# Kernel optimization log

Hardware: AMD Instinct MI355X
Metric: run time of the kernel (lower is better)

Reference implementation:

```python
import jax, jax.numpy as jnp
import numpy as np

C = 256      # channels (multiple of 32 for GroupNorm)
K = 3        # kernel
PAD = 1      # padding
G = 32       # GroupNorm groups
EPS = 1e-5


def setup_inputs() -> dict:
    key = jax.random.key(0)
    ks = jax.random.split(key, 7)
    B, H, W = 4, 64, 64
    return {
        "x": jax.random.normal(ks[0], (B, C, H, W), jnp.float32),
        "offset": jax.random.normal(ks[1], (B, 2 * K * K, H, W), jnp.float32),
        "weight": jax.random.normal(ks[2], (C, C, K, K), jnp.float32) * 0.01,
        "att_w": jax.random.normal(ks[3], (1, C), jnp.float32) * 0.01,
        "att_b": jnp.zeros((1,), jnp.float32),
        "gamma": jnp.ones((C,), jnp.float32),
        "beta": jnp.zeros((C,), jnp.float32),
    }


def _bilinear_one(xb, py, px):
    # xb: [C, H, W]; py, px: [KK, H, W] fractional sample coords (zero-pad outside)
    H, W = xb.shape[1], xb.shape[2]
    y0 = jnp.floor(py)
    x0 = jnp.floor(px)
    y1 = y0 + 1.0
    x1 = x0 + 1.0
    wy1 = py - y0
    wy0 = 1.0 - wy1
    wx1 = px - x0
    wx0 = 1.0 - wx1

    def g(yi, xi):
        valid = (yi >= 0) & (yi < H) & (xi >= 0) & (xi < W)
        yc = jnp.clip(yi, 0, H - 1).astype(jnp.int32)
        xc = jnp.clip(xi, 0, W - 1).astype(jnp.int32)
        return xb[:, yc, xc] * valid[None].astype(xb.dtype)  # [C, KK, H, W]

    return (g(y0, x0) * (wy0 * wx0)[None] + g(y0, x1) * (wy0 * wx1)[None]
            + g(y1, x0) * (wy1 * wx0)[None] + g(y1, x1) * (wy1 * wx1)[None])


def reference(x, offset, weight, att_w, att_b, gamma, beta):
    B, Cc, H, W = x.shape
    KK = K * K
    off = offset.reshape(B, KK, 2, H, W)  # (dy, dx) per kernel tap
    ii, jj = jnp.meshgrid(jnp.arange(K), jnp.arange(K), indexing='ij')
    dky = (ii - PAD).reshape(KK).astype(x.dtype)
    dkx = (jj - PAD).reshape(KK).astype(x.dtype)
    ys = jnp.arange(H, dtype=x.dtype)
    xs = jnp.arange(W, dtype=x.dtype)
    # sample coords [B, KK, H, W]
    py = ys[None, :, None] + dky[:, None, None] + off[:, :, 0]
    px = xs[None, None, :] + dkx[:, None, None] + off[:, :, 1]

    # deformable unfold: [B, C, KK, H, W]
    xu = jax.vmap(_bilinear_one)(x, py, px)

    # max over kernel taps -> channel attention gate
    xm = xu.max(axis=2)  # [B, C, H, W]
    att = jax.nn.sigmoid(jnp.einsum('bchw,oc->bohw', xm, att_w)
                         + att_b[None, :, None, None])  # [B, 1, H, W]

    # gate the unfolded samples, then emulate the conv as one GEMM
    xw = xu * att[:, :, None]  # broadcast over C, KK
    cols = xw.transpose(1, 2, 0, 3, 4).reshape(Cc * KK, B * H * W)  # [C*KK, BHW]
    out = (weight.reshape(Cc, Cc * KK) @ cols).reshape(Cc, B, H, W).transpose(1, 0, 2, 3)

    # GroupNorm(32, C) + ReLU
    og = out.reshape(B, G, Cc // G, H, W)
    mu = og.mean(axis=(2, 3, 4), keepdims=True)
    var = og.var(axis=(2, 3, 4), keepdims=True)
    on = ((og - mu) * jax.lax.rsqrt(var + EPS)).reshape(B, Cc, H, W)
    return jax.nn.relu(on * gamma[None, :, None, None] + beta[None, :, None, None])
```

## Files before the change

kernel.cpp:

```cpp
#include <hip/hip_runtime.h>

#define CT 256
#define KDIM 2304
#define COLP 296

typedef unsigned short u16;
typedef _Float16 h2 __attribute__((ext_vector_type(2)));
typedef _Float16 h8 __attribute__((ext_vector_type(8)));
typedef __attribute__((ext_vector_type(4))) float f32x4;

__device__ __forceinline__ unsigned pkh(float a, float b) {
    h2 r; r[0] = (_Float16)a; r[1] = (_Float16)b;
    return __builtin_bit_cast(unsigned, r);
}

__device__ __forceinline__ void gload_lds16(const uint4* g, u16* l) {
    __builtin_amdgcn_global_load_lds((const __attribute__((address_space(1))) void*)g,
                                     (__attribute__((address_space(3))) void*)l, 16, 0, 0);
}

__global__ __launch_bounds__(256) void k_prep(const float* __restrict__ x, uint4* __restrict__ xi,
                                              const float* __restrict__ wgt, uint4* __restrict__ pw)
{
    if (blockIdx.x < 2048) {
        int u = blockIdx.x * 256 + threadIdx.x;
        int bcg = u >> 12, p = u & 4095;
        const float* xp = x + (((size_t)bcg) << 15) + p;
        unsigned r[4];
#pragma unroll
        for (int i = 0; i < 4; ++i)
            r[i] = pkh(xp[(size_t)(2 * i) << 12], xp[(size_t)(2 * i + 1) << 12]);
        uint4 o; o.x = r[0]; o.y = r[1]; o.z = r[2]; o.w = r[3];
        xi[u] = o;
    } else {
        int u = (blockIdx.x - 2048) * 256 + threadIdx.x;
        int kc = u >> 10, rm = u & 1023;
        int m = rm >> 2, j = rm & 3;
        int round = kc / 9, tap = kc - round * 9;
        const float* src = wgt + (size_t)m * KDIM + tap;
        int c0 = round * 32 + j * 8;
        unsigned q[4];
#pragma unroll
        for (int i = 0; i < 4; ++i)
            q[i] = pkh(src[(size_t)(c0 + 2 * i) * 9], src[(size_t)(c0 + 2 * i + 1) * 9]);
        uint4 o; o.x = q[0]; o.y = q[1]; o.z = q[2]; o.w = q[3];
        pw[u] = o;
    }
}

__device__ __forceinline__ void gather_one(int it2, int sp, int xsb, size_t gfall,
                                           const uint2* s_wt, const int2* s_off,
                                           const u16* Xs, u16* col,
                                           const uint4* __restrict__ xi, int rbase, int nw)
{
    int tap = it2 >> 5, nn = it2 & 31;
    uint2 wp = s_wt[it2];
    h2 w01 = __builtin_bit_cast(h2, wp.x);
    h2 w23 = __builtin_bit_cast(h2, wp.y);
    h2 wxp = (h2){w01[0], w01[0]}, wyp = (h2){w01[1], w01[1]};
    h2 wzp = (h2){w23[0], w23[0]}, wwp = (h2){w23[1], w23[1]};
    int2 of = s_off[it2];
    int P00 = of.x & 0xffff, P01 = (of.x >> 16) & 0xffff;
    int P10 = of.y & 0xffff, P11 = (of.y >> 16) & 0xffff;
    uint4 c00, c01, c10, c11;
    int Q;
    Q = P00 - rbase;
    if ((unsigned)Q < (unsigned)nw) c00 = *(const uint4*)&Xs[xsb + Q * 8]; else c00 = xi[gfall + P00];
    Q = P01 - rbase;
    if ((unsigned)Q < (unsigned)nw) c01 = *(const uint4*)&Xs[xsb + Q * 8]; else c01 = xi[gfall + P01];
    Q = P10 - rbase;
    if ((unsigned)Q < (unsigned)nw) c10 = *(const uint4*)&Xs[xsb + Q * 8]; else c10 = xi[gfall + P10];
    Q = P11 - rbase;
    if ((unsigned)Q < (unsigned)nw) c11 = *(const uint4*)&Xs[xsb + Q * 8]; else c11 = xi[gfall + P11];
    const unsigned* a00 = (const unsigned*)&c00;
    const unsigned* a01 = (const unsigned*)&c01;
    const unsigned* a10 = (const unsigned*)&c10;
    const unsigned* a11 = (const unsigned*)&c11;
    unsigned o[4];
#pragma unroll
    for (int q = 0; q < 4; ++q) {
        h2 r = wxp * __builtin_bit_cast(h2, a00[q]) + wyp * __builtin_bit_cast(h2, a01[q])
             + wzp * __builtin_bit_cast(h2, a10[q]) + wwp * __builtin_bit_cast(h2, a11[q]);
        o[q] = __builtin_bit_cast(unsigned, r);
    }
    uint4 ov; ov.x = o[0]; ov.y = o[1]; ov.z = o[2]; ov.w = o[3];
    *(uint4*)&col[nn * COLP + tap * 32 + sp * 8] = ov;
}

__global__ __launch_bounds__(512, 2) void k_main(const uint4* __restrict__ xi, const float* __restrict__ off,
                                                 const uint4* __restrict__ pw, const float* __restrict__ att_w,
                                                 const float* __restrict__ att_b,
                                                 float* __restrict__ outp, float* __restrict__ gnpart)
{
    __shared__ uint2 s_wt[288];
    __shared__ int2 s_off[288];
    __shared__ u16 Xs[4 * 6656];
    __shared__ u16 col[32 * COLP];
    __shared__ float s_att[32];

    int rowblk = blockIdx.x >> 1, half = blockIdx.x & 1;
    int b = rowblk >> 6, h = rowblk & 63, n0 = half * 32;
    int tid = threadIdx.x;
    int lane = tid & 63, w = tid >> 6;
    int l15 = lane & 15, kb = lane >> 4;
    int wm = w * 32;
    int nn_a = w * 4 + (lane >> 4);
    int ca = (lane & 15) * 2;

    for (int e = tid; e < 288; e += 512) {
        int kk = e >> 5, wl = e & 31;
        int ww_ = n0 + wl;
        int ky = kk / 3, kx = kk - ky * 3;
        float dy = off[((size_t)(b * 18 + 2 * kk) * 64 + h) * 64 + ww_];
        float dx = off[((size_t)(b * 18 + 2 * kk + 1) * 64 + h) * 64 + ww_];
        float py = (float)(h + ky - 1) + dy;
        float px = (float)(ww_ + kx - 1) + dx;
        float y0f = floorf(py), x0f = floorf(px);
        int y0 = (int)y0f, x0 = (int)x0f;
        float fy = py - y0f, fx = px - x0f;
        float vy0 = (y0 >= 0 && y0 < 64) ? 1.f : 0.f;
        float vy1 = (y0 >= -1 && y0 < 63) ? 1.f : 0.f;
        float vx0 = (x0 >= 0 && x0 < 64) ? 1.f : 0.f;
        float vx1 = (x0 >= -1 && x0 < 63) ? 1.f : 0.f;
        float w0 = (1.f - fy) * (1.f - fx) * vy0 * vx0;
        float w1 = (1.f - fy) * fx * vy0 * vx1;
        float w2 = fy * (1.f - fx) * vy1 * vx0;
        float w3 = fy * fx * vy1 * vx1;
        uint2 wp;
        wp.x = pkh(w0, w1);
        wp.y = pkh(w2, w3);
        int yc0 = min(max(y0, 0), 63), yc1 = min(max(y0 + 1, 0), 63);
        int xc0 = min(max(x0, 0), 63), xc1 = min(max(x0 + 1, 0), 63);
        s_wt[e] = wp;
        s_off[e] = make_int2((yc0 * 64 + xc0) | ((yc0 * 64 + xc1) << 16),
                             (yc1 * 64 + xc0) | ((yc1 * 64 + xc1) << 16));
    }

    int r0 = max(0, h - 6), r1 = min(63, h + 6);
    int nrows = r1 - r0 + 1, nw = nrows * 64, rbase = r0 * 64;
    size_t xib = (size_t)(b * 32) << 12;

    float att_acc = 0.f;
    f32x4 acc[2][2];
#pragma unroll
    for (int mt = 0; mt < 2; ++mt)
#pragma unroll
        for (int nt = 0; nt < 2; ++nt) acc[mt][nt] = (f32x4){0.f, 0.f, 0.f, 0.f};

    int pwoff[2];
#pragma unroll
    for (int mt = 0; mt < 2; ++mt) pwoff[mt] = (wm + mt * 16 + l15) * 4 + kb;

#pragma unroll
    for (int cgl = 0; cgl < 2; ++cgl)
        for (int e = tid; e < nw; e += 512)
            gload_lds16(&xi[xib + ((size_t)cgl << 12) + rbase + e], &Xs[(cgl * 6656 + e * 8)]);

    for (int stage = 0; stage < 16; ++stage) {
        int buf = stage & 1;
        int s2 = stage & 1;
        __syncthreads();
        if (stage < 15) {
            size_t nb = xib + ((size_t)((stage + 1) * 2) << 12) + rbase;
#pragma unroll
            for (int cgl = 0; cgl < 2; ++cgl)
                for (int e = tid; e < nw; e += 512)
                    gload_lds16(&xi[nb + ((size_t)cgl << 12) + e],
                                &Xs[(((buf ^ 1) * 2 + cgl) * 6656 + e * 8)]);
        }
        {
            int it = tid;
            int cgl = (it >= 288) ? 1 : 0;
            gather_one(it - cgl * 288, s2 * 2 + cgl, (buf * 2 + cgl) * 6656,
                       xib + ((size_t)(stage * 2 + cgl) << 12), s_wt, s_off, Xs, col, xi, rbase, nw);
            if (tid >= 448) {
                int it2 = tid + 64;
                gather_one(it2 - 288, s2 * 2 + 1, (buf * 2 + 1) * 6656,
                           xib + ((size_t)(stage * 2 + 1) << 12), s_wt, s_off, Xs, col, xi, rbase, nw);
            }
        }

        if (stage & 1) {
            int round = stage >> 1;
            __syncthreads();

            uint4 aa[4][2];
#pragma unroll
            for (int ts = 0; ts < 4; ++ts)
#pragma unroll
                for (int mt = 0; mt < 2; ++mt)
                    aa[ts][mt] = pw[(size_t)(round * 9 + ts) * 1024 + pwoff[mt]];

            {
                int sp = ca >> 3, co = ca & 7;
                const u16* base = &col[nn_a * COLP + sp * 8 + co];
                float m0 = -1e30f, m1 = -1e30f;
#pragma unroll
                for (int t = 0; t < 9; ++t) {
                    unsigned v = *(const unsigned*)(base + t * 32);
                    h2 vv = __builtin_bit_cast(h2, v);
                    m0 = fmaxf(m0, (float)vv[0]);
                    m1 = fmaxf(m1, (float)vv[1]);
                }
                int cb = round * 32 + ca;
                att_acc += att_w[cb] * m0 + att_w[cb + 1] * m1;
            }

#pragma unroll
            for (int ts = 0; ts < 9; ++ts) {
                h8 bf[2];
#pragma unroll
                for (int nt = 0; nt < 2; ++nt)
                    bf[nt] = *(const h8*)&col[(nt * 16 + l15) * COLP + ts * 32 + kb * 8];
                h8 af[2];
#pragma unroll
                for (int mt = 0; mt < 2; ++mt) af[mt] = __builtin_bit_cast(h8, aa[ts & 3][mt]);
                if (ts + 4 < 9) {
#pragma unroll
                    for (int mt = 0; mt < 2; ++mt)
                        aa[ts & 3][mt] = pw[(size_t)(round * 9 + ts + 4) * 1024 + pwoff[mt]];
                }
#pragma unroll
                for (int mt = 0; mt < 2; ++mt)
#pragma unroll
                    for (int nt = 0; nt < 2; ++nt)
                        acc[mt][nt] = __builtin_amdgcn_mfma_f32_16x16x32_f16(af[mt], bf[nt], acc[mt][nt], 0, 0, 0);
            }
        }
    }

#pragma unroll
    for (int d = 1; d <= 8; d <<= 1) att_acc += __shfl_xor(att_acc, d);
    if ((lane & 15) == 0) s_att[nn_a] = 1.f / (1.f + expf(-(att_acc + att_b[0])));
    __syncthreads();

    float attn[2];
#pragma unroll
    for (int nt = 0; nt < 2; ++nt) attn[nt] = s_att[nt * 16 + l15];

#pragma unroll
    for (int mt = 0; mt < 2; ++mt) {
        float s1 = 0.f, s2 = 0.f;
#pragma unroll
        for (int nt = 0; nt < 2; ++nt)
#pragma unroll
            for (int r = 0; r < 4; ++r) {
                float v = acc[mt][nt][r] * attn[nt];
                int m = wm + mt * 16 + kb * 4 + r;
                outp[(((size_t)(b * CT + m)) << 12) + h * 64 + n0 + nt * 16 + l15] = v;
                s1 += v; s2 += v * v;
            }
#pragma unroll
        for (int d = 1; d <= 16; d <<= 1) {
            s1 += __shfl_xor(s1, d);
            s2 += __shfl_xor(s2, d);
        }
        if ((lane & 31) == 0) {
            int gidx = w * 4 + mt * 2 + (kb >> 1);
            gnpart[blockIdx.x * 64 + gidx * 2] = s1;
            gnpart[blockIdx.x * 64 + gidx * 2 + 1] = s2;
        }
    }
}

__global__ __launch_bounds__(256) void k_gn(const float* __restrict__ gnpart, const float* __restrict__ gamma,
                                            const float* __restrict__ beta, float* __restrict__ outp)
{
    __shared__ float rs1[128], rs2[128];
    __shared__ float s_stat[2];
    int bg = blockIdx.x;
    int b = bg >> 5, g = bg & 31;
    int tid = threadIdx.x;
    if (tid < 128) {
        int blk = (b * 64 + (tid >> 1)) * 2 + (tid & 1);
        rs1[tid] = gnpart[blk * 64 + g * 2];
        rs2[tid] = gnpart[blk * 64 + g * 2 + 1];
    }
    __syncthreads();
    if (tid < 64) {
        float a = rs1[tid] + rs1[tid + 64];
        float c = rs2[tid] + rs2[tid + 64];
#pragma unroll
        for (int d = 1; d <= 32; d <<= 1) {
            a += __shfl_xor(a, d);
            c += __shfl_xor(c, d);
        }
        if (tid == 0) {
            float mean = a * (1.f / 32768.f);
            float var = c * (1.f / 32768.f) - mean * mean;
            s_stat[0] = mean;
            s_stat[1] = rsqrtf(var + 1e-5f);
        }
    }
    __syncthreads();
    float mean = s_stat[0], rstd = s_stat[1];
    float4* p4 = (float4*)(outp + ((size_t)(b * CT + g * 8) << 12));
    for (int i = tid; i < 8192; i += 256) {
        int c = g * 8 + (i >> 10);
        float ga = gamma[c], be = beta[c];
        float4 v = p4[i];
        float4 r;
        r.x = fmaxf((v.x - mean) * rstd * ga + be, 0.f);
        r.y = fmaxf((v.y - mean) * rstd * ga + be, 0.f);
        r.z = fmaxf((v.z - mean) * rstd * ga + be, 0.f);
        r.w = fmaxf((v.w - mean) * rstd * ga + be, 0.f);
        p4[i] = r;
    }
}

extern "C" void kernel_launch(void* const* d_in, const int* in_sizes, int n_in,
                              void* d_out, int out_size, void* d_ws, size_t ws_size,
                              hipStream_t stream)
{
    const float* x = (const float*)d_in[0];
    const float* off = (const float*)d_in[1];
    const float* wgt = (const float*)d_in[2];
    const float* attw = (const float*)d_in[3];
    const float* attb = (const float*)d_in[4];
    const float* gamma = (const float*)d_in[5];
    const float* beta = (const float*)d_in[6];
    float* outp = (float*)d_out;

    char* ws = (char*)d_ws;
    uint4* xi = (uint4*)ws;
    uint4* pw = (uint4*)(ws + 8388608);
    float* gnpart = (float*)(ws + 9568256);

    k_prep<<<dim3(2336), dim3(256), 0, stream>>>(x, xi, wgt, pw);
    k_main<<<dim3(512), dim3(512), 0, stream>>>(xi, off, pw, attw, attb, outp, gnpart);
    k_gn<<<dim3(128), dim3(256), 0, stream>>>(gnpart, gamma, beta, outp);
}
```

Before: 147.1 us.

## Retile MFMA warps to 64x16 with single B fragment per step

Changes each warp's output tile from 32x32 (2x2 MFMA tiles) to 64 output channels by 16 pixels (4x1 tiles), so each step reads one column fragment from LDS but four weight fragments from global memory. Weight prefetch depth goes from 4 to 3 steps. GroupNorm partial sums are now written per 8 groups per warp with a doubled stride, and k_gn is rewritten to reduce 128 partials per group with wave shuffles. This trades LDS reads for more global weight loads and more registers.

```diff
diff --git a/kernel.cpp b/kernel.cpp
--- a/kernel.cpp
+++ b/kernel.cpp
@@ -103,7 +103,8 @@
     int tid = threadIdx.x;
     int lane = tid & 63, w = tid >> 6;
     int l15 = lane & 15, kb = lane >> 4;
-    int wm = w * 32;
+    int wm = (w & 3) * 64;
+    int nt_w = w >> 2;
     int nn_a = w * 4 + (lane >> 4);
     int ca = (lane & 15) * 2;
 
@@ -141,15 +142,14 @@
     size_t xib = (size_t)(b * 32) << 12;
 
     float att_acc = 0.f;
-    f32x4 acc[2][2];
-#pragma unroll
-    for (int mt = 0; mt < 2; ++mt)
-#pragma unroll
-        for (int nt = 0; nt < 2; ++nt) acc[mt][nt] = (f32x4){0.f, 0.f, 0.f, 0.f};
-
-    int pwoff[2];
-#pragma unroll
-    for (int mt = 0; mt < 2; ++mt) pwoff[mt] = (wm + mt * 16 + l15) * 4 + kb;
+    f32x4 acc[4];
+#pragma unroll
+    for (int mt = 0; mt < 4; ++mt) acc[mt] = (f32x4){0.f, 0.f, 0.f, 0.f};
+
+    int pwoff[4];
+#pragma unroll
+    for (int mt = 0; mt < 4; ++mt) pwoff[mt] = (wm + mt * 16 + l15) * 4 + kb;
+    int bcol = (nt_w * 16 + l15) * COLP + kb * 8;
 
 #pragma unroll
     for (int cgl = 0; cgl < 2; ++cgl)
@@ -184,11 +184,11 @@
             int round = stage >> 1;
             __syncthreads();
 
-            uint4 aa[4][2];
-#pragma unroll
-            for (int ts = 0; ts < 4; ++ts)
-#pragma unroll
-                for (int mt = 0; mt < 2; ++mt)
+            uint4 aa[3][4];
+#pragma unroll
+            for (int ts = 0; ts < 3; ++ts)
+#pragma unroll
+                for (int mt = 0; mt < 4; ++mt)
                     aa[ts][mt] = pw[(size_t)(round * 9 + ts) * 1024 + pwoff[mt]];
 
             {
@@ -208,23 +208,18 @@
 
 #pragma unroll
             for (int ts = 0; ts < 9; ++ts) {
-                h8 bf[2];
-#pragma unroll
-                for (int nt = 0; nt < 2; ++nt)
-                    bf[nt] = *(const h8*)&col[(nt * 16 + l15) * COLP + ts * 32 + kb * 8];
-                h8 af[2];
-#pragma unroll
-                for (int mt = 0; mt < 2; ++mt) af[mt] = __builtin_bit_cast(h8, aa[ts & 3][mt]);
-                if (ts + 4 < 9) {
-#pragma unroll
-                    for (int mt = 0; mt < 2; ++mt)
-                        aa[ts & 3][mt] = pw[(size_t)(round * 9 + ts + 4) * 1024 + pwoff[mt]];
+                h8 bf = *(const h8*)&col[bcol + ts * 32];
+                h8 af[4];
+#pragma unroll
+                for (int mt = 0; mt < 4; ++mt) af[mt] = __builtin_bit_cast(h8, aa[ts % 3][mt]);
+                if (ts + 3 < 9) {
+#pragma unroll
+                    for (int mt = 0; mt < 4; ++mt)
+                        aa[ts % 3][mt] = pw[(size_t)(round * 9 + ts + 3) * 1024 + pwoff[mt]];
                 }
 #pragma unroll
-                for (int mt = 0; mt < 2; ++mt)
-#pragma unroll
-                    for (int nt = 0; nt < 2; ++nt)
-                        acc[mt][nt] = __builtin_amdgcn_mfma_f32_16x16x32_f16(af[mt], bf[nt], acc[mt][nt], 0, 0, 0);
+                for (int mt = 0; mt < 4; ++mt)
+                    acc[mt] = __builtin_amdgcn_mfma_f32_16x16x32_f16(af[mt], bf, acc[mt], 0, 0, 0);
             }
         }
     }
@@ -234,31 +229,27 @@
     if ((lane & 15) == 0) s_att[nn_a] = 1.f / (1.f + expf(-(att_acc + att_b[0])));
     __syncthreads();
 
-    float attn[2];
-#pragma unroll
-    for (int nt = 0; nt < 2; ++nt) attn[nt] = s_att[nt * 16 + l15];
-
-#pragma unroll
-    for (int mt = 0; mt < 2; ++mt) {
+    float attn = s_att[nt_w * 16 + l15];
+
+#pragma unroll
+    for (int mt = 0; mt < 4; ++mt) {
         float s1 = 0.f, s2 = 0.f;
 #pragma unroll
-        for (int nt = 0; nt < 2; ++nt)
-#pragma unroll
-            for (int r = 0; r < 4; ++r) {
-                float v = acc[mt][nt][r] * attn[nt];
-                int m = wm + mt * 16 + kb * 4 + r;
-                outp[(((size_t)(b * CT + m)) << 12) + h * 64 + n0 + nt * 16 + l15] = v;
-                s1 += v; s2 += v * v;
-            }
+        for (int r = 0; r < 4; ++r) {
+            float v = acc[mt][r] * attn;
+            int m = wm + mt * 16 + kb * 4 + r;
+            outp[(((size_t)(b * CT + m)) << 12) + h * 64 + n0 + nt_w * 16 + l15] = v;
+            s1 += v; s2 += v * v;
+        }
 #pragma unroll
         for (int d = 1; d <= 16; d <<= 1) {
             s1 += __shfl_xor(s1, d);
             s2 += __shfl_xor(s2, d);
         }
         if ((lane & 31) == 0) {
-            int gidx = w * 4 + mt * 2 + (kb >> 1);
-            gnpart[blockIdx.x * 64 + gidx * 2] = s1;
-            gnpart[blockIdx.x * 64 + gidx * 2 + 1] = s2;
+            int gidx = w * 8 + mt * 2 + (kb >> 1);
+            gnpart[(size_t)blockIdx.x * 128 + gidx * 2] = s1;
+            gnpart[(size_t)blockIdx.x * 128 + gidx * 2 + 1] = s2;
         }
     }
 }
@@ -266,38 +257,39 @@
 __global__ __launch_bounds__(256) void k_gn(const float* __restrict__ gnpart, const float* __restrict__ gamma,
                                             const float* __restrict__ beta, float* __restrict__ outp)
 {
-    __shared__ float rs1[128], rs2[128];
+    __shared__ float rs1[4], rs2[4];
     __shared__ float s_stat[2];
     int bg = blockIdx.x;
     int b = bg >> 5, g = bg & 31;
     int tid = threadIdx.x;
-    if (tid < 128) {
-        int blk = (b * 64 + (tid >> 1)) * 2 + (tid & 1);
-        rs1[tid] = gnpart[blk * 64 + g * 2];
-        rs2[tid] = gnpart[blk * 64 + g * 2 + 1];
-    }
+    float a, c;
+    {
+        int blkloc = tid & 127, wsel = tid >> 7;
+        int gidx = (g >> 3) * 8 + ((g >> 1) & 3) * 2 + (g & 1) + wsel * 32;
+        const float* p = &gnpart[((size_t)(b * 128 + blkloc)) * 128 + gidx * 2];
+        a = p[0]; c = p[1];
+    }
+#pragma unroll
+    for (int d = 1; d <= 32; d <<= 1) {
+        a += __shfl_xor(a, d);
+        c += __shfl_xor(c, d);
+    }
+    if ((tid & 63) == 0) { rs1[tid >> 6] = a; rs2[tid >> 6] = c; }
     __syncthreads();
-    if (tid < 64) {
-        float a = rs1[tid] + rs1[tid + 64];
-        float c = rs2[tid] + rs2[tid + 64];
-#pragma unroll
-        for (int d = 1; d <= 32; d <<= 1) {
-            a += __shfl_xor(a, d);
-            c += __shfl_xor(c, d);
-        }
-        if (tid == 0) {
-            float mean = a * (1.f / 32768.f);
-            float var = c * (1.f / 32768.f) - mean * mean;
-            s_stat[0] = mean;
-            s_stat[1] = rsqrtf(var + 1e-5f);
-        }
+    if (tid == 0) {
+        float S1 = rs1[0] + rs1[1] + rs1[2] + rs1[3];
+        float S2 = rs2[0] + rs2[1] + rs2[2] + rs2[3];
+        float mean = S1 * (1.f / 32768.f);
+        float var = S2 * (1.f / 32768.f) - mean * mean;
+        s_stat[0] = mean;
+        s_stat[1] = rsqrtf(var + 1e-5f);
     }
     __syncthreads();
     float mean = s_stat[0], rstd = s_stat[1];
     float4* p4 = (float4*)(outp + ((size_t)(b * CT + g * 8) << 12));
     for (int i = tid; i < 8192; i += 256) {
-        int c = g * 8 + (i >> 10);
-        float ga = gamma[c], be = beta[c];
+        int c2 = g * 8 + (i >> 10);
+        float ga = gamma[c2], be = beta[c2];
         float4 v = p4[i];
         float4 r;
         r.x = fmaxf((v.x - mean) * rstd * ga + be, 0.f);
```

Result: slower. 180.4 us (+22.7%).
